# Performance work log

Measured on AMD Instinct MI355X. Metric: run time of the kernel, lower is better.

The kernel has to match this reference:

```python
import jax, jax.numpy as jnp
import numpy as np

D_MODEL = 1024
NUM_HEADS = 16
D_K = D_MODEL // NUM_HEADS
B, S = 4, 2048


def setup_inputs() -> dict:
    key = jax.random.key(0)
    ks = jax.random.split(key, 11)
    scale = 1.0 / np.sqrt(D_MODEL)
    inp = {
        'query': jax.random.normal(ks[0], (B, S, D_MODEL), dtype=jnp.float32),
        'key':   jax.random.normal(ks[1], (B, S, D_MODEL), dtype=jnp.float32),
        'value': jax.random.normal(ks[2], (B, S, D_MODEL), dtype=jnp.float32),
        'Wq': jax.random.normal(ks[3], (D_MODEL, D_MODEL), dtype=jnp.float32) * scale,
        'bq': jnp.zeros((D_MODEL,), dtype=jnp.float32),
        'Wk': jax.random.normal(ks[4], (D_MODEL, D_MODEL), dtype=jnp.float32) * scale,
        'bk': jnp.zeros((D_MODEL,), dtype=jnp.float32),
        'Wv': jax.random.normal(ks[5], (D_MODEL, D_MODEL), dtype=jnp.float32) * scale,
        'bv': jnp.zeros((D_MODEL,), dtype=jnp.float32),
        'Wo': jax.random.normal(ks[6], (D_MODEL, D_MODEL), dtype=jnp.float32) * scale,
        'bo': jnp.zeros((D_MODEL,), dtype=jnp.float32),
    }
    return inp


def reference(query, key, value, Wq, bq, Wk, bk, Wv, bv, Wo, bo):
    b, sq, _ = query.shape
    sk = key.shape[1]
    # projections (torch Linear: x @ W.T + b; here W stored as [in, out])
    Q = query @ Wq + bq
    K = key @ Wk + bk
    V = value @ Wv + bv
    # split heads: [b, h, s, d_k]
    Q = Q.reshape(b, sq, NUM_HEADS, D_K).transpose(0, 2, 1, 3)
    K = K.reshape(b, sk, NUM_HEADS, D_K).transpose(0, 2, 1, 3)
    V = V.reshape(b, sk, NUM_HEADS, D_K).transpose(0, 2, 1, 3)
    # scaled dot-product attention (full [b,h,sq,sk] scores, as in source)
    scores = jnp.einsum('bhqd,bhkd->bhqk', Q, K) / jnp.sqrt(jnp.float32(D_K))
    attn = jax.nn.softmax(scores, axis=-1)
    out = jnp.einsum('bhqk,bhkd->bhqd', attn, V)
    out = out.transpose(0, 2, 1, 3).reshape(b, sq, D_MODEL)
    return out @ Wo + bo
```

## Files before the change

### kernel.cpp

```cpp
#include <hip/hip_runtime.h>
#include <hip/hip_bf16.h>
#include <stdint.h>

typedef __bf16 bf16x8 __attribute__((ext_vector_type(8)));
typedef __bf16 bf16x4 __attribute__((ext_vector_type(4)));
typedef float  f32x4  __attribute__((ext_vector_type(4)));
typedef unsigned short u16;

#define D_MODEL 1024
#define NUM_HEADS 16
#define DK 64
#define BATCH 4
#define SEQ 2048
#define M_TOTAL (BATCH*SEQ)
#define QK_SCALE 0.18033688011112042f

static __device__ __forceinline__ u16 f2bf(float f) {
    __bf16 h = (__bf16)f;
    return __builtin_bit_cast(u16, h);
}

#define ASYNC16(gptr, lptr) __builtin_amdgcn_global_load_lds( \
    (const __attribute__((address_space(1))) unsigned*)(uintptr_t)(gptr), \
    (__attribute__((address_space(3))) unsigned*)(unsigned)(uintptr_t)(lptr), 16, 0, 0)

#define FENCE() asm volatile("" ::: "memory")
#define BARRIER() do { FENCE(); __builtin_amdgcn_s_barrier(); FENCE(); } while (0)

__global__ void detect_dtype(const u16* __restrict__ q, unsigned* __restrict__ flag) {
    __shared__ int sh[256];
    int cnt = 0;
    for (int i = threadIdx.x; i < 8192; i += 256) {
        u16 v = q[2 * i];
        int e = (v >> 7) & 0xFF;
        if (e >= 100 && e <= 134) cnt++;
    }
    sh[threadIdx.x] = cnt;
    __syncthreads();
    for (int s = 128; s > 0; s >>= 1) {
        if (threadIdx.x < s) sh[threadIdx.x] += sh[threadIdx.x + s];
        __syncthreads();
    }
    if (threadIdx.x == 0) *flag = (sh[0] > 4096) ? 1u : 0u;
}

__global__ void transpose_w(const u16* __restrict__ W0, const u16* __restrict__ W1,
                            const u16* __restrict__ W2, const u16* __restrict__ W3,
                            u16* __restrict__ WT, const unsigned* __restrict__ flagp) {
    __shared__ u16 tile[32][33];
    const u16* W = (blockIdx.z == 0) ? W0 : (blockIdx.z == 1) ? W1 : (blockIdx.z == 2) ? W2 : W3;
    u16* T = WT + (size_t)blockIdx.z * D_MODEL * D_MODEL;
    bool is_bf16 = (*flagp != 0);
    int x = threadIdx.x, y0 = threadIdx.y;
    int bx = blockIdx.x * 32, by = blockIdx.y * 32;
    if (is_bf16) {
#pragma unroll
        for (int i = 0; i < 4; i++) {
            int y = y0 + i * 8;
            tile[y][x] = W[(size_t)(by + y) * D_MODEL + bx + x];
        }
    } else {
        const float* Wf = (const float*)W;
#pragma unroll
        for (int i = 0; i < 4; i++) {
            int y = y0 + i * 8;
            tile[y][x] = f2bf(Wf[(size_t)(by + y) * D_MODEL + bx + x]);
        }
    }
    __syncthreads();
#pragma unroll
    for (int i = 0; i < 4; i++) {
        int y = y0 + i * 8;
        T[(size_t)(bx + y) * D_MODEL + by + x] = tile[x][y];
    }
}

__global__ __launch_bounds__(512, 2) void gemm_qkv(
    const u16* __restrict__ qin, const u16* __restrict__ kin, const u16* __restrict__ vin,
    const u16* __restrict__ WT,
    const u16* __restrict__ bq, const u16* __restrict__ bk, const u16* __restrict__ bv,
    u16* __restrict__ Qp, u16* __restrict__ Kp, u16* __restrict__ VpT,
    const unsigned* __restrict__ flagp)
{
    __shared__ __align__(16) u16 As[2][256 * 64];
    __shared__ __align__(16) u16 Bs[2][256 * 64];

    const int KTILES = D_MODEL / 64;

    const int id  = blockIdx.x;
    const int wg  = (id & 7) * 48 + (id >> 3);
    const int z   = wg >> 7;
    const int rr  = wg & 127;
    const int m_blk = (rr >> 2) * 256;
    const int n_blk = (rr & 3) * 256;

    const u16* A    = (z == 0) ? qin : (z == 1) ? kin : vin;
    const u16* W    = WT + (size_t)z * 1048576;
    const u16* bias = (z == 0) ? bq : (z == 1) ? bk : bv;
    u16* C          = (z == 0) ? Qp : (z == 1) ? Kp : VpT;
    const float oscale = (z == 0) ? QK_SCALE : 1.0f;
    const bool is_bf16 = (*flagp != 0);
    const float* Af = (const float*)A;

    const int tid  = threadIdx.x;
    const int lane = tid & 63, w = tid >> 6;
    const int quad = lane >> 4, l15 = lane & 15;
    const int swz  = l15 & 7;
    const int wm = w >> 2, wn = w & 3;

    const int lrow = lane >> 3;
    const int ug   = (lane & 7) ^ lrow;

    auto stageA = [&](int t, int h) {
        if (t >= KTILES) return;
        u16* ldsbase = &As[t & 1][h * 8192];
        const int k0 = t * 64;
#pragma unroll
        for (int i = 0; i < 2; i++) {
            const int c   = w * 2 + i;
            const int row = m_blk + h * 128 + c * 8 + lrow;
            if (is_bf16) {
                ASYNC16(A + (size_t)row * D_MODEL + k0 + ug * 8, ldsbase + c * 512);
            } else {
                const float* s = Af + (size_t)row * D_MODEL + k0 + ug * 8;
                float4 f0 = ((const float4*)s)[0];
                float4 f1 = ((const float4*)s)[1];
                bf16x8 p;
                p[0] = (__bf16)f0.x; p[1] = (__bf16)f0.y; p[2] = (__bf16)f0.z; p[3] = (__bf16)f0.w;
                p[4] = (__bf16)f1.x; p[5] = (__bf16)f1.y; p[6] = (__bf16)f1.z; p[7] = (__bf16)f1.w;
                *(bf16x8*)(ldsbase + c * 512 + lane * 8) = p;
            }
        }
    };
    auto stageB = [&](int t, int h) {
        if (t >= KTILES) return;
        u16* ldsbase = &Bs[t & 1][h * 8192];
        const int k0 = t * 64;
#pragma unroll
        for (int i = 0; i < 2; i++) {
            const int c   = w * 2 + i;
            const int row = n_blk + h * 128 + c * 8 + lrow;
            ASYNC16(W + (size_t)row * D_MODEL + k0 + ug * 8, ldsbase + c * 512);
        }
    };

    f32x4 acc[8][4] = {};
    bf16x8 a[4][2];
    bf16x8 b[4][2];

#define LOAD_A(MBASE) \
    _Pragma("unroll") \
    for (int mf = 0; mf < 4; mf++) \
        _Pragma("unroll") \
        for (int ks = 0; ks < 2; ks++) \
            a[mf][ks] = *(const bf16x8*)&Abuf[(wm * 128 + (MBASE + mf) * 16 + l15) * 64 \
                                              + (((ks * 4 + quad) ^ swz) * 8)];
#define LOAD_B(NBASE) \
    _Pragma("unroll") \
    for (int nf = 0; nf < 2; nf++) \
        _Pragma("unroll") \
        for (int ks = 0; ks < 2; ks++) \
            b[NBASE + nf][ks] = *(const bf16x8*)&Bbuf[(wn * 64 + (NBASE + nf) * 16 + l15) * 64 \
                                                      + (((ks * 4 + quad) ^ swz) * 8)];
#define MFMA_QUAD(MBASE, NBASE) \
    __builtin_amdgcn_s_setprio(1); \
    _Pragma("unroll") \
    for (int mf = 0; mf < 4; mf++) \
        _Pragma("unroll") \
        for (int nf = 0; nf < 2; nf++) \
            _Pragma("unroll") \
            for (int ks = 0; ks < 2; ks++) \
                acc[MBASE + mf][NBASE + nf] = __builtin_amdgcn_mfma_f32_16x16x32_bf16( \
                    a[mf][ks], b[NBASE + nf][ks], acc[MBASE + mf][NBASE + nf], 0, 0, 0); \
    __builtin_amdgcn_s_setprio(0);

    stageB(0, 0); stageB(0, 1);
    stageA(0, 0); stageA(0, 1);
    stageB(1, 0); stageB(1, 1);
    asm volatile("s_waitcnt vmcnt(4) lgkmcnt(0)" ::: "memory");
    __builtin_amdgcn_s_barrier();
    FENCE();

#pragma unroll 1
    for (int t = 0; t < KTILES; t++) {
        const u16* Abuf = &As[t & 1][0];
        const u16* Bbuf = &Bs[t & 1][0];

        LOAD_A(0); LOAD_B(0);
        stageA(t + 1, 0);
        BARRIER();
        asm volatile("s_waitcnt lgkmcnt(0)" ::: "memory");
        MFMA_QUAD(0, 0);
        BARRIER();

        LOAD_B(2);
        stageA(t + 1, 1);
        BARRIER();
        asm volatile("s_waitcnt lgkmcnt(0)" ::: "memory");
        MFMA_QUAD(0, 2);
        BARRIER();

        LOAD_A(4);
        stageB(t + 2, 0);
        BARRIER();
        asm volatile("s_waitcnt lgkmcnt(0)" ::: "memory");
        MFMA_QUAD(4, 2);
        BARRIER();

        stageB(t + 2, 1);
        BARRIER();
        asm volatile("s_waitcnt lgkmcnt(0)" ::: "memory");
        MFMA_QUAD(4, 0);
        if (t == KTILES - 2)      { asm volatile("s_waitcnt vmcnt(0)" ::: "memory"); }
        else if (t < KTILES - 2)  { asm volatile("s_waitcnt vmcnt(4)" ::: "memory"); }
        BARRIER();
    }
#undef LOAD_A
#undef LOAD_B
#undef MFMA_QUAD

#pragma unroll
    for (int nf = 0; nf < 4; nf++) {
        const int n = n_blk + wn * 64 + nf * 16 + l15;
        const float bvf = is_bf16 ? (float)((const __bf16*)bias)[n] : ((const float*)bias)[n];
#pragma unroll
        for (int mf = 0; mf < 8; mf++) {
            const int mrow = m_blk + wm * 128 + mf * 16 + quad * 4;
            if (z == 2) {
                const int bb = mrow >> 11, s = mrow & 2047;
                ushort4 pk;
                pk.x = f2bf(acc[mf][nf][0] + bvf);
                pk.y = f2bf(acc[mf][nf][1] + bvf);
                pk.z = f2bf(acc[mf][nf][2] + bvf);
                pk.w = f2bf(acc[mf][nf][3] + bvf);
                *(ushort4*)(C + (size_t)bb * D_MODEL * SEQ + (size_t)n * SEQ + s) = pk;
            } else {
#pragma unroll
                for (int r = 0; r < 4; r++)
                    C[(size_t)(mrow + r) * D_MODEL + n] = f2bf((acc[mf][nf][r] + bvf) * oscale);
            }
        }
    }
}

__global__ __launch_bounds__(256) void gemm_o(
    const u16* __restrict__ A, const u16* __restrict__ WT,
    const u16* __restrict__ bias, u16* __restrict__ C,
    const unsigned* __restrict__ flagp)
{
    __shared__ __align__(16) u16 As[64 * 32];
    __shared__ __align__(16) u16 Bs[128 * 32];
    const int id  = blockIdx.x;
    const int xcd = id & 7, j = id >> 3;
    const int by  = xcd * 16 + (j >> 3);
    const int bx  = j & 7;

    const int tid  = threadIdx.x;
    const int lane = tid & 63, w = tid >> 6;
    const int quad = lane >> 4, l15 = lane & 15;
    const int wm = w >> 1, wn = w & 1;
    const int m_blk = by * 64, n_blk = bx * 128;
    const bool is_bf16 = (*flagp != 0);

    f32x4 acc[2][4] = {};
    const int srow = lane >> 2, skp = (lane & 3) * 8;

    for (int k0 = 0; k0 < D_MODEL; k0 += 32) {
#pragma unroll
        for (int i = 0; i < 3; i++) {
            int c = w * 3 + i;
            if (c < 4)
                ASYNC16(A  + (size_t)(m_blk + c * 16 + srow) * D_MODEL + k0 + skp, &As[c * 512]);
            else
                ASYNC16(WT + (size_t)(n_blk + (c - 4) * 16 + srow) * D_MODEL + k0 + skp, &Bs[(c - 4) * 512]);
        }
        __syncthreads();

        bf16x8 af[2], bg[4];
#pragma unroll
        for (int sm = 0; sm < 2; sm++)
            af[sm] = *(const bf16x8*)&As[(wm * 32 + sm * 16 + l15) * 32 + quad * 8];
#pragma unroll
        for (int sn = 0; sn < 4; sn++)
            bg[sn] = *(const bf16x8*)&Bs[(wn * 64 + sn * 16 + l15) * 32 + quad * 8];
#pragma unroll
        for (int sm = 0; sm < 2; sm++)
#pragma unroll
            for (int sn = 0; sn < 4; sn++)
                acc[sm][sn] = __builtin_amdgcn_mfma_f32_16x16x32_bf16(af[sm], bg[sn], acc[sm][sn], 0, 0, 0);
        __syncthreads();
    }

#pragma unroll
    for (int sn = 0; sn < 4; sn++) {
        int n = n_blk + wn * 64 + sn * 16 + l15;
        float bvf = is_bf16 ? (float)((const __bf16*)bias)[n] : ((const float*)bias)[n];
#pragma unroll
        for (int sm = 0; sm < 2; sm++) {
            int mrow = m_blk + wm * 32 + sm * 16 + quad * 4;
            if (!is_bf16) {
                float* Cf = (float*)C;
#pragma unroll
                for (int r = 0; r < 4; r++)
                    Cf[(size_t)(mrow + r) * D_MODEL + n] = acc[sm][sn][r] + bvf;
            } else {
#pragma unroll
                for (int r = 0; r < 4; r++)
                    C[(size_t)(mrow + r) * D_MODEL + n] = f2bf(acc[sm][sn][r] + bvf);
            }
        }
    }
}

__global__ __launch_bounds__(256) void attn_kernel(
    const u16* __restrict__ Qp, const u16* __restrict__ Kp,
    const u16* __restrict__ VpT, u16* __restrict__ AO)
{
    __shared__ __align__(16) u16 Ks[2][64 * 64];
    __shared__ __align__(16) u16 Vs[2][64 * 64];
    __shared__ __align__(16) u16 Ps[4][32][68];
    const int id  = blockIdx.x;
    const int xcd = id & 7, j = id >> 3;
    const int bh  = xcd * 8 + (j >> 4);
    const int qx  = j & 15;

    const int tid  = threadIdx.x;
    const int lane = tid & 63, w = tid >> 6;
    const int quad = lane >> 4, l15 = lane & 15;
    const int b = bh >> 4, h = bh & 15;
    const int q_base = qx * 128 + w * 32;

    bf16x8 bQ[2][2];
#pragma unroll
    for (int sn = 0; sn < 2; sn++)
#pragma unroll
        for (int ds = 0; ds < 2; ds++)
            bQ[sn][ds] = *(const bf16x8*)(Qp + (size_t)(b * SEQ + q_base + sn * 16 + l15) * D_MODEL
                                              + h * DK + ds * 32 + quad * 8);

    float lsum[2] = {0.0f, 0.0f};
    f32x4 OT[2][4] = {};

    const u16* Kbase = Kp  + (size_t)(b * SEQ) * D_MODEL + h * DK;
    const u16* Vbase = VpT + (size_t)b * D_MODEL * SEQ + (size_t)(h * DK) * SEQ;

    const int c0   = w * 2;
    const int lrow = lane >> 3;
    const int ug   = (lane & 7) ^ lrow;
    const int swz  = l15 & 7;

    auto issue_tile = [&](int key0, int bf) {
#pragma unroll
        for (int i = 0; i < 2; i++) {
            int c = c0 + i;
            ASYNC16(Kbase + (size_t)(key0 + c * 8 + lrow) * D_MODEL + ug * 8, &Ks[bf][c * 512]);
            ASYNC16(Vbase + (size_t)(c * 8 + lrow) * SEQ + key0 + ug * 8,     &Vs[bf][c * 512]);
        }
    };

    issue_tile(0, 0);
    __syncthreads();

    for (int t = 0; t < SEQ / 64; t++) {
        const int cur = t & 1;
        if (t + 1 < SEQ / 64) issue_tile((t + 1) * 64, cur ^ 1);

#pragma unroll
        for (int kc = 0; kc < 4; kc++) {
            const int krow = (kc * 16 + l15) * 64;
            bf16x8 k0 = *(const bf16x8*)&Ks[cur][krow + ((quad ^ swz) * 8)];
            bf16x8 k1 = *(const bf16x8*)&Ks[cur][krow + (((4 + quad) ^ swz) * 8)];
#pragma unroll
            for (int sn = 0; sn < 2; sn++) {
                f32x4 s = {};
                s = __builtin_amdgcn_mfma_f32_16x16x32_bf16(k0, bQ[sn][0], s, 0, 0, 0);
                s = __builtin_amdgcn_mfma_f32_16x16x32_bf16(k1, bQ[sn][1], s, 0, 0, 0);
                float p0 = __builtin_amdgcn_exp2f(s[0]);
                float p1 = __builtin_amdgcn_exp2f(s[1]);
                float p2 = __builtin_amdgcn_exp2f(s[2]);
                float p3 = __builtin_amdgcn_exp2f(s[3]);
                lsum[sn] += (p0 + p1) + (p2 + p3);
                bf16x4 pk;
                pk[0] = (__bf16)p0; pk[1] = (__bf16)p1; pk[2] = (__bf16)p2; pk[3] = (__bf16)p3;
                *(bf16x4*)&Ps[w][sn * 16 + l15][kc * 16 + quad * 4] = pk;
            }
        }

#pragma unroll
        for (int kc2 = 0; kc2 < 2; kc2++) {
            bf16x8 bP0 = *(const bf16x8*)&Ps[w][l15][kc2 * 32 + quad * 8];
            bf16x8 bP1 = *(const bf16x8*)&Ps[w][16 + l15][kc2 * 32 + quad * 8];
#pragma unroll
            for (int nd = 0; nd < 4; nd++) {
                bf16x8 aV = *(const bf16x8*)&Vs[cur][(nd * 16 + l15) * 64
                                                    + (((kc2 * 4 + quad) ^ swz) * 8)];
                OT[0][nd] = __builtin_amdgcn_mfma_f32_16x16x32_bf16(aV, bP0, OT[0][nd], 0, 0, 0);
                OT[1][nd] = __builtin_amdgcn_mfma_f32_16x16x32_bf16(aV, bP1, OT[1][nd], 0, 0, 0);
            }
        }
        __syncthreads();
    }

#pragma unroll
    for (int sn = 0; sn < 2; sn++) {
        lsum[sn] += __shfl_xor(lsum[sn], 16, 64);
        lsum[sn] += __shfl_xor(lsum[sn], 32, 64);
        float rl = 1.0f / lsum[sn];
        size_t rowbase = (size_t)(b * SEQ + q_base + sn * 16 + l15) * D_MODEL + h * DK;
#pragma unroll
        for (int nd = 0; nd < 4; nd++) {
            ushort4 pk;
            pk.x = f2bf(OT[sn][nd][0] * rl);
            pk.y = f2bf(OT[sn][nd][1] * rl);
            pk.z = f2bf(OT[sn][nd][2] * rl);
            pk.w = f2bf(OT[sn][nd][3] * rl);
            *(ushort4*)(AO + rowbase + nd * 16 + quad * 4) = pk;
        }
    }
}

extern "C" void kernel_launch(void* const* d_in, const int* in_sizes, int n_in,
                              void* d_out, int out_size, void* d_ws, size_t ws_size,
                              hipStream_t stream) {
    const u16* q  = (const u16*)d_in[0];
    const u16* k  = (const u16*)d_in[1];
    const u16* v  = (const u16*)d_in[2];
    const u16* Wq = (const u16*)d_in[3];
    const u16* bq = (const u16*)d_in[4];
    const u16* Wk = (const u16*)d_in[5];
    const u16* bk = (const u16*)d_in[6];
    const u16* Wv = (const u16*)d_in[7];
    const u16* bv = (const u16*)d_in[8];
    const u16* Wo = (const u16*)d_in[9];
    const u16* bo = (const u16*)d_in[10];

    u16* ws   = (u16*)d_ws;
    unsigned* flagp = (unsigned*)ws;
    u16* WT   = ws + 16;
    u16* Qp   = WT + (size_t)4 * 1024 * 1024;
    u16* Kp   = Qp + (size_t)M_TOTAL * D_MODEL;
    u16* VpT  = Kp + (size_t)M_TOTAL * D_MODEL;
    u16* AO   = VpT + (size_t)M_TOTAL * D_MODEL;

    detect_dtype<<<1, 256, 0, stream>>>(q, flagp);
    transpose_w<<<dim3(32, 32, 4), dim3(32, 8), 0, stream>>>(Wq, Wk, Wv, Wo, WT, flagp);
    gemm_qkv<<<384, 512, 0, stream>>>(q, k, v, WT, bq, bk, bv, Qp, Kp, VpT, flagp);
    attn_kernel<<<1024, 256, 0, stream>>>(Qp, Kp, VpT, AO);
    gemm_o<<<1024, 256, 0, stream>>>(AO, WT + 3 * 1048576, bo, (u16*)d_out, flagp);
}
```

Before: 443.2 us.

## Shrink QKV GEMM tile to 256x128 and register-stage A loads

Halves the QKV projection tile width to 256x128, doubling the grid to 768 workgroups with an 8x... wave layout of 4x2 and fewer accumulators per thread. The A operand is now loaded into registers one phase early and written to LDS later, replacing async global-to-LDS copies and in-loop fp32 conversion stalls, so global latency overlaps MFMA work. The aim is better CU occupancy and load balance across the 256 CUs. The cost is lower arithmetic intensity per tile, more redundant A reads, and more register pressure from the staged loads.

```diff
diff --git a/kernel.cpp b/kernel.cpp
--- a/kernel.cpp
+++ b/kernel.cpp
@@ -83,16 +83,16 @@
     const unsigned* __restrict__ flagp)
 {
     __shared__ __align__(16) u16 As[2][256 * 64];
-    __shared__ __align__(16) u16 Bs[2][256 * 64];
+    __shared__ __align__(16) u16 Bs[2][128 * 64];
 
     const int KTILES = D_MODEL / 64;
 
     const int id  = blockIdx.x;
-    const int wg  = (id & 7) * 48 + (id >> 3);
-    const int z   = wg >> 7;
-    const int rr  = wg & 127;
-    const int m_blk = (rr >> 2) * 256;
-    const int n_blk = (rr & 3) * 256;
+    const int wg  = (id & 7) * 96 + (id >> 3);
+    const int z   = wg >> 8;
+    const int rr  = wg & 255;
+    const int m_blk = (rr >> 3) * 256;
+    const int n_blk = (rr & 7) * 128;
 
     const u16* A    = (z == 0) ? qin : (z == 1) ? kin : vin;
     const u16* W    = WT + (size_t)z * 1048576;
@@ -106,78 +106,91 @@
     const int lane = tid & 63, w = tid >> 6;
     const int quad = lane >> 4, l15 = lane & 15;
     const int swz  = l15 & 7;
-    const int wm = w >> 2, wn = w & 3;
+    const int wm = w >> 1, wn = w & 1;
 
     const int lrow = lane >> 3;
     const int ug   = (lane & 7) ^ lrow;
 
-    auto stageA = [&](int t, int h) {
+    auto stageB = [&](int t) {
         if (t >= KTILES) return;
-        u16* ldsbase = &As[t & 1][h * 8192];
+        u16* lb = &Bs[t & 1][0];
         const int k0 = t * 64;
 #pragma unroll
         for (int i = 0; i < 2; i++) {
             const int c   = w * 2 + i;
-            const int row = m_blk + h * 128 + c * 8 + lrow;
-            if (is_bf16) {
-                ASYNC16(A + (size_t)row * D_MODEL + k0 + ug * 8, ldsbase + c * 512);
-            } else {
-                const float* s = Af + (size_t)row * D_MODEL + k0 + ug * 8;
-                float4 f0 = ((const float4*)s)[0];
-                float4 f1 = ((const float4*)s)[1];
-                bf16x8 p;
-                p[0] = (__bf16)f0.x; p[1] = (__bf16)f0.y; p[2] = (__bf16)f0.z; p[3] = (__bf16)f0.w;
-                p[4] = (__bf16)f1.x; p[5] = (__bf16)f1.y; p[6] = (__bf16)f1.z; p[7] = (__bf16)f1.w;
-                *(bf16x8*)(ldsbase + c * 512 + lane * 8) = p;
-            }
+            const int row = n_blk + c * 8 + lrow;
+            ASYNC16(W + (size_t)row * D_MODEL + k0 + ug * 8, lb + c * 512);
         }
     };
-    auto stageB = [&](int t, int h) {
-        if (t >= KTILES) return;
-        u16* ldsbase = &Bs[t & 1][h * 8192];
-        const int k0 = t * 64;
-#pragma unroll
-        for (int i = 0; i < 2; i++) {
-            const int c   = w * 2 + i;
-            const int row = n_blk + h * 128 + c * 8 + lrow;
-            ASYNC16(W + (size_t)row * D_MODEL + k0 + ug * 8, ldsbase + c * 512);
-        }
-    };
-
-    f32x4 acc[8][4] = {};
-    bf16x8 a[4][2];
+
+    float4 fa0[4], fa1[4];
+    uint4  ua0[2], ua1[2];
+
+#define ISSUE_A(T, H) do { if ((T) < KTILES) { \
+    _Pragma("unroll") \
+    for (int i_ = 0; i_ < 2; i_++) { \
+        const int c_ = w * 2 + i_; \
+        const size_t row_ = (size_t)(m_blk + (H) * 128 + c_ * 8 + lrow); \
+        if (is_bf16) { \
+            ua##H[i_] = *(const uint4*)(A + row_ * D_MODEL + (T) * 64 + ug * 8); \
+        } else { \
+            const float* s_ = Af + row_ * D_MODEL + (T) * 64 + ug * 8; \
+            fa##H[i_ * 2]     = ((const float4*)s_)[0]; \
+            fa##H[i_ * 2 + 1] = ((const float4*)s_)[1]; \
+        } \
+    } } } while (0)
+
+#define WRITE_A(T, H) do { if ((T) < KTILES) { \
+    u16* lb_ = &As[(T) & 1][(H) * 8192]; \
+    _Pragma("unroll") \
+    for (int i_ = 0; i_ < 2; i_++) { \
+        const int c_ = w * 2 + i_; \
+        if (is_bf16) { \
+            *(uint4*)(lb_ + c_ * 512 + lane * 8) = ua##H[i_]; \
+        } else { \
+            bf16x8 p_; \
+            float4 f0_ = fa##H[i_ * 2], f1_ = fa##H[i_ * 2 + 1]; \
+            p_[0] = (__bf16)f0_.x; p_[1] = (__bf16)f0_.y; p_[2] = (__bf16)f0_.z; p_[3] = (__bf16)f0_.w; \
+            p_[4] = (__bf16)f1_.x; p_[5] = (__bf16)f1_.y; p_[6] = (__bf16)f1_.z; p_[7] = (__bf16)f1_.w; \
+            *(bf16x8*)(lb_ + c_ * 512 + lane * 8) = p_; \
+        } \
+    } } } while (0)
+
+    f32x4 acc[4][4] = {};
+    bf16x8 a[2][2];
     bf16x8 b[4][2];
 
 #define LOAD_A(MBASE) \
     _Pragma("unroll") \
-    for (int mf = 0; mf < 4; mf++) \
+    for (int mf = 0; mf < 2; mf++) \
         _Pragma("unroll") \
         for (int ks = 0; ks < 2; ks++) \
-            a[mf][ks] = *(const bf16x8*)&Abuf[(wm * 128 + (MBASE + mf) * 16 + l15) * 64 \
+            a[mf][ks] = *(const bf16x8*)&Abuf[(size_t)(wm * 64 + ((MBASE) + mf) * 16 + l15) * 64 \
                                               + (((ks * 4 + quad) ^ swz) * 8)];
 #define LOAD_B(NBASE) \
     _Pragma("unroll") \
     for (int nf = 0; nf < 2; nf++) \
         _Pragma("unroll") \
         for (int ks = 0; ks < 2; ks++) \
-            b[NBASE + nf][ks] = *(const bf16x8*)&Bbuf[(wn * 64 + (NBASE + nf) * 16 + l15) * 64 \
-                                                      + (((ks * 4 + quad) ^ swz) * 8)];
-#define MFMA_QUAD(MBASE, NBASE) \
+            b[(NBASE) + nf][ks] = *(const bf16x8*)&Bbuf[(size_t)(wn * 64 + ((NBASE) + nf) * 16 + l15) * 64 \
+                                                        + (((ks * 4 + quad) ^ swz) * 8)];
+#define MFMA8(MBASE, NBASE) \
     __builtin_amdgcn_s_setprio(1); \
     _Pragma("unroll") \
-    for (int mf = 0; mf < 4; mf++) \
+    for (int mf = 0; mf < 2; mf++) \
         _Pragma("unroll") \
         for (int nf = 0; nf < 2; nf++) \
             _Pragma("unroll") \
             for (int ks = 0; ks < 2; ks++) \
-                acc[MBASE + mf][NBASE + nf] = __builtin_amdgcn_mfma_f32_16x16x32_bf16( \
-                    a[mf][ks], b[NBASE + nf][ks], acc[MBASE + mf][NBASE + nf], 0, 0, 0); \
+                acc[(MBASE) + mf][(NBASE) + nf] = __builtin_amdgcn_mfma_f32_16x16x32_bf16( \
+                    a[mf][ks], b[(NBASE) + nf][ks], acc[(MBASE) + mf][(NBASE) + nf], 0, 0, 0); \
     __builtin_amdgcn_s_setprio(0);
 
-    stageB(0, 0); stageB(0, 1);
-    stageA(0, 0); stageA(0, 1);
-    stageB(1, 0); stageB(1, 1);
-    asm volatile("s_waitcnt vmcnt(4) lgkmcnt(0)" ::: "memory");
+    stageB(0);
+    ISSUE_A(0, 0); ISSUE_A(0, 1);
+    stageB(1);
+    WRITE_A(0, 0); WRITE_A(0, 1);
+    asm volatile("s_waitcnt vmcnt(2) lgkmcnt(0)" ::: "memory");
     __builtin_amdgcn_s_barrier();
     FENCE();
 
@@ -187,45 +200,48 @@
         const u16* Bbuf = &Bs[t & 1][0];
 
         LOAD_A(0); LOAD_B(0);
-        stageA(t + 1, 0);
+        ISSUE_A(t + 1, 0);
         BARRIER();
         asm volatile("s_waitcnt lgkmcnt(0)" ::: "memory");
-        MFMA_QUAD(0, 0);
+        MFMA8(0, 0);
         BARRIER();
 
         LOAD_B(2);
-        stageA(t + 1, 1);
+        ISSUE_A(t + 1, 1);
         BARRIER();
         asm volatile("s_waitcnt lgkmcnt(0)" ::: "memory");
-        MFMA_QUAD(0, 2);
-        BARRIER();
-
-        LOAD_A(4);
-        stageB(t + 2, 0);
+        MFMA8(0, 2);
+        BARRIER();
+
+        LOAD_A(2);
+        stageB(t + 2);
+        WRITE_A(t + 1, 0);
         BARRIER();
         asm volatile("s_waitcnt lgkmcnt(0)" ::: "memory");
-        MFMA_QUAD(4, 2);
-        BARRIER();
-
-        stageB(t + 2, 1);
+        MFMA8(2, 2);
+        BARRIER();
+
+        WRITE_A(t + 1, 1);
         BARRIER();
         asm volatile("s_waitcnt lgkmcnt(0)" ::: "memory");
-        MFMA_QUAD(4, 0);
+        MFMA8(2, 0);
         if (t == KTILES - 2)      { asm volatile("s_waitcnt vmcnt(0)" ::: "memory"); }
-        else if (t < KTILES - 2)  { asm volatile("s_waitcnt vmcnt(4)" ::: "memory"); }
+        else if (t < KTILES - 2)  { asm volatile("s_waitcnt vmcnt(2)" ::: "memory"); }
         BARRIER();
     }
 #undef LOAD_A
 #undef LOAD_B
-#undef MFMA_QUAD
+#undef MFMA8
+#undef ISSUE_A
+#undef WRITE_A
 
 #pragma unroll
     for (int nf = 0; nf < 4; nf++) {
         const int n = n_blk + wn * 64 + nf * 16 + l15;
         const float bvf = is_bf16 ? (float)((const __bf16*)bias)[n] : ((const float*)bias)[n];
 #pragma unroll
-        for (int mf = 0; mf < 8; mf++) {
-            const int mrow = m_blk + wm * 128 + mf * 16 + quad * 4;
+        for (int mf = 0; mf < 4; mf++) {
+            const int mrow = m_blk + wm * 64 + mf * 16 + quad * 4;
             if (z == 2) {
                 const int bb = mrow >> 11, s = mrow & 2047;
                 ushort4 pk;
@@ -444,7 +460,7 @@
 
     detect_dtype<<<1, 256, 0, stream>>>(q, flagp);
     transpose_w<<<dim3(32, 32, 4), dim3(32, 8), 0, stream>>>(Wq, Wk, Wv, Wo, WT, flagp);
-    gemm_qkv<<<384, 512, 0, stream>>>(q, k, v, WT, bq, bk, bv, Qp, Kp, VpT, flagp);
+    gemm_qkv<<<768, 512, 0, stream>>>(q, k, v, WT, bq, bk, bv, Qp, Kp, VpT, flagp);
     attn_kernel<<<1024, 256, 0, stream>>>(Qp, Kp, VpT, AO);
     gemm_o<<<1024, 256, 0, stream>>>(AO, WT + 3 * 1048576, bo, (u16*)d_out, flagp);
 }
```

After: 475.4 us. +7.3%, slower.
